# Kernel optimization log

Measured on AMD Instinct MI355X. Metric: run time of the kernel, lower is better.

## Reference

```python
import jax, jax.numpy as jnp
import numpy as np

DIM = 768
HEADS = 12
TOPK = 32


def setup_inputs() -> dict:
    key = jax.random.key(0)
    k1, k2, k3 = jax.random.split(key, 3)
    B, hw, T = 8, 576, 4
    N = hw + T * hw
    x = jax.random.normal(k1, (B, N, DIM), dtype=jnp.float32)
    qkv_w = jax.random.normal(k2, (3 * DIM, DIM), dtype=jnp.float32) * 0.02
    proj_w = jax.random.normal(k3, (DIM, DIM), dtype=jnp.float32) * 0.02
    proj_b = jnp.zeros((DIM,), dtype=jnp.float32)
    return {"x": x, "qkv_w": qkv_w, "proj_w": proj_w, "proj_b": proj_b, "T": T, "hw": hw}


def _query_topk_every_frame(attn, hw, T):
    # attn: [B, H, hw, hw + T*hw]
    B, H, n1, _ = attn.shape
    qa = attn[..., :hw]                       # [B,H,hw,hw] query self part
    ma = attn[..., hw:].reshape(B, H, n1, T, hw)  # per-frame memory scores
    vals, idx = jax.lax.top_k(ma, TOPK)       # [B,H,hw,T,K]
    cat = jnp.concatenate([qa, vals.reshape(B, H, n1, T * TOPK)], axis=-1)
    sm = jax.nn.softmax(cat, axis=-1)         # softmax over hw + T*K survivors
    qa2 = sm[..., :hw]
    tv = sm[..., hw:].reshape(B, H, n1, T, TOPK)
    # scatter normalized top-k values back into dense per-frame affinity
    bi = jnp.arange(B)[:, None, None, None, None]
    hi = jnp.arange(H)[None, :, None, None, None]
    ni = jnp.arange(n1)[None, None, :, None, None]
    ti = jnp.arange(T)[None, None, None, :, None]
    aff = jnp.zeros_like(ma).at[bi, hi, ni, ti, idx].set(tv)
    return jnp.concatenate([qa2, aff.reshape(B, H, n1, T * hw)], axis=-1)


def reference(x, qkv_w, proj_w, proj_b, T, hw):
    B, N, C = x.shape
    assert N == hw + T * hw
    hd = C // HEADS
    scale = hd ** -0.5
    qkv = (x @ qkv_w.T).reshape(B, N, 3, HEADS, hd).transpose(2, 0, 3, 1, 4)
    q, k, v = qkv[0], qkv[1], qkv[2]          # each [B,H,N,hd]
    query_q = q[:, :, :hw]                    # [B,H,hw,hd]
    attn = jnp.einsum('bhqd,bhkd->bhqk', query_q, k) * scale  # [B,H,hw,N]
    attn = _query_topk_every_frame(attn, hw, T)
    out = jnp.einsum('bhqk,bhkd->bhqd', attn, v)  # [B,H,hw,hd]
    query = out.transpose(0, 2, 1, 3).reshape(B, hw, C)
    query = query @ proj_w.T + proj_b
    # memory tokens pass through unchanged
    return jnp.concatenate([query, x[:, hw:]], axis=1)
```

## Files before the change

kernel.cpp:

```cpp
#include <hip/hip_runtime.h>
#include <hip/hip_bf16.h>


using s16x8 = __attribute__((ext_vector_type(8))) short;
using f32x4 = __attribute__((ext_vector_type(4))) float;
typedef unsigned short u16;

#define MFMA_B16(A,B,C) __builtin_amdgcn_mfma_f32_16x16x32_bf16(A,B,C,0,0,0)

__device__ __forceinline__ u16 f2bf(float f) {
  unsigned u = __float_as_uint(f);
  u += 0x7FFFu + ((u >> 16) & 1u);
  return (u16)(u >> 16);
}
__device__ __forceinline__ float bf2f(u16 h) {
  return __uint_as_float(((unsigned)h) << 16);
}
__device__ __forceinline__ int lanes_below(unsigned long long m) {
  return __builtin_amdgcn_mbcnt_hi((unsigned)(m >> 32),
         __builtin_amdgcn_mbcnt_lo((unsigned)m, 0));
}

__global__ __launch_bounds__(256) void cvt_kernel(const float* __restrict__ src,
                                                  u16* __restrict__ dst, int n4) {
  int i = blockIdx.x * blockDim.x + threadIdx.x;
  if (i >= n4) return;
  float4 v = ((const float4*)src)[i];
  unsigned lo = (unsigned)f2bf(v.x) | ((unsigned)f2bf(v.y) << 16);
  unsigned hi = (unsigned)f2bf(v.z) | ((unsigned)f2bf(v.w) << 16);
  uint2 o; o.x = lo; o.y = hi;
  ((uint2*)dst)[i] = o;
}

__global__ __launch_bounds__(256) void copy_tail_kernel(const float* __restrict__ x,
                                                        float* __restrict__ out) {
  int i = blockIdx.x * blockDim.x + threadIdx.x;
  int b = i / 442368;
  int off = i - b * 442368;
  size_t e = (size_t)b * 552960 + 110592 + off;
  ((float4*)out)[e] = ((const float4*)x)[e];
}

template<int MODE>
__global__ __launch_bounds__(256) void gemm_nt(
    const u16* __restrict__ A, const u16* __restrict__ Bw,
    const float* __restrict__ bias,
    u16* __restrict__ qbuf, u16* __restrict__ kbuf,
    u16* __restrict__ vbuf, u16* __restrict__ vtb,
    float* __restrict__ fout)
{
  constexpr int LDT = 72;
  __shared__ __align__(16) u16 sA[64 * LDT];
  __shared__ __align__(16) u16 sB[64 * LDT];
  const int n0 = blockIdx.x * 64;
  const int m0 = blockIdx.y * 64;
  if (MODE == 0) {
    if (n0 < 768 && (blockIdx.y % 45) >= 9) return;
  }
  const int tid = threadIdx.x;
  const int w = tid >> 6, lane = tid & 63;
  const int srow = tid >> 2, scb = tid & 3;
  const int mh = (w >> 1) * 32, nh = (w & 1) * 32;
  f32x4 z = {0.f, 0.f, 0.f, 0.f};
  f32x4 acc[2][2] = {{z, z}, {z, z}};

  for (int k0 = 0; k0 < 768; k0 += 64) {
    __syncthreads();
    #pragma unroll
    for (int c = scb; c < 8; c += 4) {
      *(int4*)&sA[srow * LDT + c * 8] =
          *(const int4*)&A[(size_t)(m0 + srow) * 768 + k0 + c * 8];
      *(int4*)&sB[srow * LDT + c * 8] =
          *(const int4*)&Bw[(size_t)(n0 + srow) * 768 + k0 + c * 8];
    }
    __syncthreads();
    #pragma unroll
    for (int kk = 0; kk < 2; ++kk) {
      const int ko = kk * 32 + (lane >> 4) * 8;
      s16x8 a0 = *(const s16x8*)&sA[(mh +      (lane & 15)) * LDT + ko];
      s16x8 a1 = *(const s16x8*)&sA[(mh + 16 + (lane & 15)) * LDT + ko];
      s16x8 b0 = *(const s16x8*)&sB[(nh +      (lane & 15)) * LDT + ko];
      s16x8 b1 = *(const s16x8*)&sB[(nh + 16 + (lane & 15)) * LDT + ko];
      acc[0][0] = MFMA_B16(a0, b0, acc[0][0]);
      acc[0][1] = MFMA_B16(a0, b1, acc[0][1]);
      acc[1][0] = MFMA_B16(a1, b0, acc[1][0]);
      acc[1][1] = MFMA_B16(a1, b1, acc[1][1]);
    }
  }

  if (MODE == 0) {
    const int which = n0 / 768;
    const int h = (n0 % 768) >> 6;
    #pragma unroll
    for (int mi = 0; mi < 2; ++mi)
      #pragma unroll
      for (int ni = 0; ni < 2; ++ni)
        #pragma unroll
        for (int r = 0; r < 4; ++r) {
          const int gm = m0 + mh + mi * 16 + (lane >> 4) * 4 + r;
          const int d  = nh + ni * 16 + (lane & 15);
          const int b  = gm / 2880;
          const int rr = gm - b * 2880;
          const float c = acc[mi][ni][r];
          if (which == 0) {
            if (rr < 576)
              qbuf[((size_t)(b * 12 + h) * 576 + rr) * 64 + d] = f2bf(c * 0.125f);
          } else if (which == 1) {
            kbuf[((size_t)(b * 12 + h) * 2880 + rr) * 64 + d] = f2bf(c);
          } else {
            const u16 bv = f2bf(c);
            vbuf[((size_t)(b * 12 + h) * 2880 + rr) * 64 + d] = bv;
            vtb[((size_t)((b * 12 + h) * 64 + d)) * 2880 + rr] = bv;
          }
        }
  } else {
    #pragma unroll
    for (int mi = 0; mi < 2; ++mi)
      #pragma unroll
      for (int ni = 0; ni < 2; ++ni)
        #pragma unroll
        for (int r = 0; r < 4; ++r) {
          const int gm = m0 + mh + mi * 16 + (lane >> 4) * 4 + r;
          const int gn = n0 + nh + ni * 16 + (lane & 15);
          const int b = gm / 576;
          const int q = gm - b * 576;
          fout[((size_t)b * 2880 + q) * 768 + gn] = acc[mi][ni][r] + bias[gn];
        }
  }
}

__global__ __launch_bounds__(256, 8) void attn_kernel(
    const u16* __restrict__ qbuf, const u16* __restrict__ kbuf,
    const u16* __restrict__ vbuf, const u16* __restrict__ vtb,
    u16* __restrict__ aout)
{
  constexpr int PST = 584;
  __shared__ __align__(16) u16 s_p[16 * PST];
  __shared__ float s_denom[16];

  const int bid = blockIdx.x;
  const int L = (bid & 7) * 432 + (bid >> 3);
  const int qt = L % 36;
  const int h  = (L / 36) % 12;
  const int b  = L / 432;
  const int bh = b * 12 + h;
  const int q0 = qt * 16;
  const int tid = threadIdx.x, w = tid >> 6, lane = tid & 63;
  const int l15 = lane & 15, rg = lane >> 4;
  const int ko = rg * 8;

  const u16* qp = qbuf + ((size_t)bh * 576 + q0) * 64;
  s16x8 aQ[2];
  aQ[0] = *(const s16x8*)&qp[l15 * 64 + ko];
  aQ[1] = *(const s16x8*)&qp[l15 * 64 + 32 + ko];

  const u16* kp = kbuf + (size_t)bh * 2880 * 64;
  const u16* vt = vtb + ((size_t)bh * 64 + w * 16 + l15) * 2880;
  f32x4 zz = {0.f, 0.f, 0.f, 0.f};
  f32x4 accO = zz;

  for (int c = 0; c < 5; ++c) {
    #pragma unroll 3
    for (int t = 0; t < 9; ++t) {
      const int wk = w * 144 + t * 16;
      const u16* kr = kp + (size_t)(c * 576 + wk + l15) * 64 + ko;
      s16x8 kf0 = *(const s16x8*)&kr[0];
      s16x8 kf1 = *(const s16x8*)&kr[32];
      f32x4 a0 = zz;
      a0 = MFMA_B16(aQ[0], kf0, a0);
      a0 = MFMA_B16(aQ[1], kf1, a0);
      if (c == 0) {
        #pragma unroll
        for (int r = 0; r < 4; ++r)
          s_p[(rg * 4 + r) * PST + wk + l15] = f2bf(__expf(a0[r]));
      } else {
        #pragma unroll
        for (int r = 0; r < 4; ++r)
          s_p[(rg * 4 + r) * PST + wk + l15] = f2bf(a0[r]);
      }
    }
    __syncthreads();

    if (c == 0) {
      #pragma unroll
      for (int ri = 0; ri < 4; ++ri) {
        const int q = w * 4 + ri;
        float s = 0.f;
        #pragma unroll
        for (int j = 0; j < 9; ++j) s += bf2f(s_p[q * PST + lane + 64 * j]);
        #pragma unroll
        for (int off = 1; off < 64; off <<= 1) s += __shfl_xor(s, off);
        if (lane == 0) s_denom[q] = s;
      }
    } else {
      for (int ri = 0; ri < 4; ++ri) {
        const int q = w * 4 + ri;
        unsigned key[9];
        #pragma unroll
        for (int j = 0; j < 9; ++j) {
          unsigned raw = s_p[q * PST + lane + 64 * j];
          key[j] = (raw & 0x8000u) ? (raw ^ 0xFFFFu) : (raw | 0x8000u);
        }
        unsigned prefix = 0;
        for (int bit = 15; bit >= 0; --bit) {
          const unsigned cand = prefix | (1u << bit);
          int cnt = 0;
          #pragma unroll
          for (int j = 0; j < 9; ++j)
            cnt += __popcll(__ballot(key[j] >= cand));
          if (cnt >= 32) prefix = cand;
          if (cnt == 32) break;
        }
        unsigned long long eqm[9];
        int cnt_gt = 0;
        #pragma unroll
        for (int j = 0; j < 9; ++j) {
          cnt_gt += __popcll(__ballot(key[j] > prefix));
          eqm[j] = __ballot(key[j] == prefix);
        }
        const int rem = 32 - cnt_gt;
        int run_eq = 0;
        float dsum = 0.f;
        #pragma unroll
        for (int j = 0; j < 9; ++j) {
          const unsigned kk = key[j];
          const bool sel = (kk > prefix) ||
              (kk == prefix && run_eq + lanes_below(eqm[j]) < rem);
          const u16 raw = (kk & 0x8000u) ? (u16)(kk ^ 0x8000u) : (u16)(kk ^ 0xFFFFu);
          const float e = __expf(bf2f(raw));
          const float p = sel ? e : 0.f;
          dsum += p;
          s_p[q * PST + lane + 64 * j] = f2bf(p);
          run_eq += __popcll(eqm[j]);
        }
        #pragma unroll
        for (int off = 1; off < 64; off <<= 1) dsum += __shfl_xor(dsum, off);
        if (lane == 0) s_denom[q] += dsum;
      }
      __syncthreads();
    }

    #pragma unroll 3
    for (int k0 = 0; k0 < 576; k0 += 32) {
      s16x8 vf = *(const s16x8*)&vt[c * 576 + k0 + ko];
      s16x8 pa = *(const s16x8*)&s_p[l15 * PST + k0 + ko];
      accO = MFMA_B16(pa, vf, accO);
    }
    __syncthreads();
  }

  const int d = w * 16 + l15;
  #pragma unroll
  for (int r = 0; r < 4; ++r) {
    const int row = rg * 4 + r;
    const float val = accO[r] / s_denom[row];
    aout[((size_t)(b * 576 + q0 + row)) * 768 + h * 64 + d] = f2bf(val);
  }
}

extern "C" void kernel_launch(void* const* d_in, const int* in_sizes, int n_in,
                              void* d_out, int out_size, void* d_ws, size_t ws_size,
                              hipStream_t stream)
{
  const float* x      = (const float*)d_in[0];
  const float* qkv_w  = (const float*)d_in[1];
  const float* proj_w = (const float*)d_in[2];
  const float* proj_b = (const float*)d_in[3];
  float* out = (float*)d_out;

  char* ws = (char*)d_ws;
  size_t off = 0;
  auto alloc = [&](size_t bytes) -> void* {
    void* p = ws + off;
    off += (bytes + 255) & ~(size_t)255;
    return p;
  };
  u16* xb   = (u16*)alloc((size_t)23040 * 768 * 2);
  u16* wqb  = (u16*)alloc((size_t)2304 * 768 * 2);
  u16* wpb  = (u16*)alloc((size_t)768 * 768 * 2);
  u16* qbuf = (u16*)alloc((size_t)96 * 576 * 64 * 2);
  u16* vtb  = (u16*)alloc((size_t)96 * 64 * 2880 * 2);
  u16* aout = (u16*)alloc((size_t)4608 * 768 * 2);
  u16* kbuf = (u16*)d_out;
  u16* vbuf = kbuf + (size_t)96 * 2880 * 64;

  cvt_kernel<<<17280, 256, 0, stream>>>(x, xb, 17694720 / 4);
  cvt_kernel<<<1728, 256, 0, stream>>>(qkv_w, wqb, 1769472 / 4);
  cvt_kernel<<<576, 256, 0, stream>>>(proj_w, wpb, 589824 / 4);
  gemm_nt<0><<<dim3(36, 360), 256, 0, stream>>>(xb, wqb, nullptr,
                                                qbuf, kbuf, vbuf, vtb, nullptr);
  attn_kernel<<<3456, 256, 0, stream>>>(qbuf, kbuf, vbuf, vtb, aout);
  gemm_nt<1><<<dim3(12, 72), 256, 0, stream>>>(aout, wpb, proj_b,
                                               nullptr, nullptr, nullptr, nullptr, out);
  copy_tail_kernel<<<13824, 256, 0, stream>>>(x, out);
}
```

Before: 533.8 us.

## Enlarge GEMM tiles with direct-to-LDS loads, split V transpose, streamline top-k

The GEMM moves from 64x64 to 128x128 tiles with 4x4 MFMA per wave and stages operands through global_load_lds, which raises data reuse and cuts register round-trips. The strided transposed-V store in the QKV epilogue becomes a separate LDS-based transpose kernel. The attention kernel now exponentiates every score before top-k, since exp is monotonic and positive, so keys need no sign handling. It also processes two rows per radix-select pass with no early exit and uses a permuted LDS row layout. The tradeoffs are an extra launch, more register pressure and an unpadded 64-wide LDS stride that may cause bank conflicts.

```diff
diff --git a/kernel.cpp b/kernel.cpp
--- a/kernel.cpp
+++ b/kernel.cpp
@@ -19,6 +19,11 @@
 __device__ __forceinline__ int lanes_below(unsigned long long m) {
   return __builtin_amdgcn_mbcnt_hi((unsigned)(m >> 32),
          __builtin_amdgcn_mbcnt_lo((unsigned)m, 0));
+}
+__device__ __forceinline__ void stage16(const u16* __restrict__ g, u16* l) {
+  __builtin_amdgcn_global_load_lds(
+      (const __attribute__((address_space(1))) unsigned int*)g,
+      (__attribute__((address_space(3))) unsigned int*)l, 16, 0, 0);
 }
 
 __global__ __launch_bounds__(256) void cvt_kernel(const float* __restrict__ src,
@@ -41,66 +46,96 @@
   ((float4*)out)[e] = ((const float4*)x)[e];
 }
 
+__global__ __launch_bounds__(256) void transpose_v(const u16* __restrict__ vbuf,
+                                                   u16* __restrict__ vtb) {
+  __shared__ __align__(16) u16 s[64][72];
+  const int r0 = blockIdx.x * 64;
+  const int bh = blockIdx.y;
+  const int t = threadIdx.x;
+  const int kr = t >> 2, c0 = (t & 3) * 16;
+  const u16* src = vbuf + (size_t)bh * 2880 * 64 + (size_t)(r0 + kr) * 64 + c0;
+  *(int4*)&s[kr][c0]     = *(const int4*)&src[0];
+  *(int4*)&s[kr][c0 + 8] = *(const int4*)&src[8];
+  __syncthreads();
+  const int d = t >> 2, k0 = (t & 3) * 16;
+  u16 tmp[16];
+  #pragma unroll
+  for (int i = 0; i < 16; ++i) tmp[i] = s[k0 + i][d];
+  u16* dst = vtb + ((size_t)bh * 64 + d) * 2880 + r0 + k0;
+  *(int4*)&dst[0] = *(const int4*)&tmp[0];
+  *(int4*)&dst[8] = *(const int4*)&tmp[8];
+}
+
 template<int MODE>
 __global__ __launch_bounds__(256) void gemm_nt(
     const u16* __restrict__ A, const u16* __restrict__ Bw,
     const float* __restrict__ bias,
     u16* __restrict__ qbuf, u16* __restrict__ kbuf,
-    u16* __restrict__ vbuf, u16* __restrict__ vtb,
-    float* __restrict__ fout)
+    u16* __restrict__ vbuf, float* __restrict__ fout)
 {
-  constexpr int LDT = 72;
-  __shared__ __align__(16) u16 sA[64 * LDT];
-  __shared__ __align__(16) u16 sB[64 * LDT];
-  const int n0 = blockIdx.x * 64;
-  const int m0 = blockIdx.y * 64;
-  if (MODE == 0) {
-    if (n0 < 768 && (blockIdx.y % 45) >= 9) return;
+  __shared__ __align__(16) u16 sA[128 * 64];
+  __shared__ __align__(16) u16 sB[128 * 64];
+  const int n0 = blockIdx.x * 128;
+  const int m0 = blockIdx.y * 128;
+  if (MODE == 0 && n0 < 768) {
+    const int s = m0 % 2880;
+    if (s >= 576 && s + 128 <= 2880) return;
   }
   const int tid = threadIdx.x;
   const int w = tid >> 6, lane = tid & 63;
-  const int srow = tid >> 2, scb = tid & 3;
-  const int mh = (w >> 1) * 32, nh = (w & 1) * 32;
+  const int l15 = lane & 15, rg = lane >> 4;
+  const int ko = rg * 8;
+  const int mq = (w >> 1) * 64, nq = (w & 1) * 64;
+  const int trow = tid >> 3, tcol = (tid & 7) * 8;
+
   f32x4 z = {0.f, 0.f, 0.f, 0.f};
-  f32x4 acc[2][2] = {{z, z}, {z, z}};
+  f32x4 acc[4][4];
+  #pragma unroll
+  for (int i = 0; i < 4; ++i)
+    #pragma unroll
+    for (int j = 0; j < 4; ++j) acc[i][j] = z;
 
   for (int k0 = 0; k0 < 768; k0 += 64) {
     __syncthreads();
     #pragma unroll
-    for (int c = scb; c < 8; c += 4) {
-      *(int4*)&sA[srow * LDT + c * 8] =
-          *(const int4*)&A[(size_t)(m0 + srow) * 768 + k0 + c * 8];
-      *(int4*)&sB[srow * LDT + c * 8] =
-          *(const int4*)&Bw[(size_t)(n0 + srow) * 768 + k0 + c * 8];
+    for (int i = 0; i < 4; ++i) {
+      stage16(&A[(size_t)(m0 + trow + i * 32) * 768 + k0 + tcol],
+              &sA[(trow + i * 32) * 64 + tcol]);
+      stage16(&Bw[(size_t)(n0 + trow + i * 32) * 768 + k0 + tcol],
+              &sB[(trow + i * 32) * 64 + tcol]);
     }
     __syncthreads();
     #pragma unroll
     for (int kk = 0; kk < 2; ++kk) {
-      const int ko = kk * 32 + (lane >> 4) * 8;
-      s16x8 a0 = *(const s16x8*)&sA[(mh +      (lane & 15)) * LDT + ko];
-      s16x8 a1 = *(const s16x8*)&sA[(mh + 16 + (lane & 15)) * LDT + ko];
-      s16x8 b0 = *(const s16x8*)&sB[(nh +      (lane & 15)) * LDT + ko];
-      s16x8 b1 = *(const s16x8*)&sB[(nh + 16 + (lane & 15)) * LDT + ko];
-      acc[0][0] = MFMA_B16(a0, b0, acc[0][0]);
-      acc[0][1] = MFMA_B16(a0, b1, acc[0][1]);
-      acc[1][0] = MFMA_B16(a1, b0, acc[1][0]);
-      acc[1][1] = MFMA_B16(a1, b1, acc[1][1]);
+      const int ko2 = kk * 32 + ko;
+      s16x8 af[4], bf[4];
+      #pragma unroll
+      for (int i = 0; i < 4; ++i) {
+        af[i] = *(const s16x8*)&sA[(mq + i * 16 + l15) * 64 + ko2];
+        bf[i] = *(const s16x8*)&sB[(nq + i * 16 + l15) * 64 + ko2];
+      }
+      #pragma unroll
+      for (int mi = 0; mi < 4; ++mi)
+        #pragma unroll
+        for (int ni = 0; ni < 4; ++ni)
+          acc[mi][ni] = MFMA_B16(af[mi], bf[ni], acc[mi][ni]);
     }
   }
 
   if (MODE == 0) {
     const int which = n0 / 768;
-    const int h = (n0 % 768) >> 6;
-    #pragma unroll
-    for (int mi = 0; mi < 2; ++mi)
-      #pragma unroll
-      for (int ni = 0; ni < 2; ++ni)
+    const int nb = n0 % 768;
+    #pragma unroll
+    for (int mi = 0; mi < 4; ++mi)
+      #pragma unroll
+      for (int ni = 0; ni < 4; ++ni)
         #pragma unroll
         for (int r = 0; r < 4; ++r) {
-          const int gm = m0 + mh + mi * 16 + (lane >> 4) * 4 + r;
-          const int d  = nh + ni * 16 + (lane & 15);
+          const int gm = m0 + mq + mi * 16 + rg * 4 + r;
           const int b  = gm / 2880;
           const int rr = gm - b * 2880;
+          const int ng = nb + nq + ni * 16 + l15;
+          const int h  = ng >> 6, d = ng & 63;
           const float c = acc[mi][ni][r];
           if (which == 0) {
             if (rr < 576)
@@ -108,20 +143,18 @@
           } else if (which == 1) {
             kbuf[((size_t)(b * 12 + h) * 2880 + rr) * 64 + d] = f2bf(c);
           } else {
-            const u16 bv = f2bf(c);
-            vbuf[((size_t)(b * 12 + h) * 2880 + rr) * 64 + d] = bv;
-            vtb[((size_t)((b * 12 + h) * 64 + d)) * 2880 + rr] = bv;
+            vbuf[((size_t)(b * 12 + h) * 2880 + rr) * 64 + d] = f2bf(c);
           }
         }
   } else {
     #pragma unroll
-    for (int mi = 0; mi < 2; ++mi)
-      #pragma unroll
-      for (int ni = 0; ni < 2; ++ni)
+    for (int mi = 0; mi < 4; ++mi)
+      #pragma unroll
+      for (int ni = 0; ni < 4; ++ni)
         #pragma unroll
         for (int r = 0; r < 4; ++r) {
-          const int gm = m0 + mh + mi * 16 + (lane >> 4) * 4 + r;
-          const int gn = n0 + nh + ni * 16 + (lane & 15);
+          const int gm = m0 + mq + mi * 16 + rg * 4 + r;
+          const int gn = n0 + nq + ni * 16 + l15;
           const int b = gm / 576;
           const int q = gm - b * 576;
           fout[((size_t)b * 2880 + q) * 768 + gn] = acc[mi][ni][r] + bias[gn];
@@ -131,8 +164,7 @@
 
 __global__ __launch_bounds__(256, 8) void attn_kernel(
     const u16* __restrict__ qbuf, const u16* __restrict__ kbuf,
-    const u16* __restrict__ vbuf, const u16* __restrict__ vtb,
-    u16* __restrict__ aout)
+    const u16* __restrict__ vtb, u16* __restrict__ aout)
 {
   constexpr int PST = 584;
   __shared__ __align__(16) u16 s_p[16 * PST];
@@ -156,8 +188,63 @@
 
   const u16* kp = kbuf + (size_t)bh * 2880 * 64;
   const u16* vt = vtb + ((size_t)bh * 64 + w * 16 + l15) * 2880;
+  const int prow = (((l15 & 3) << 2) | (l15 >> 2)) * PST;
   f32x4 zz = {0.f, 0.f, 0.f, 0.f};
   f32x4 accO = zz;
+
+  auto writeback = [&](int q, int lrow, const unsigned* k, unsigned prefix) {
+    unsigned long long eqm[9];
+    int cnt_gt = 0;
+    #pragma unroll
+    for (int j = 0; j < 9; ++j) {
+      unsigned long long ge = __ballot(k[j] >= prefix);
+      unsigned long long gt = __ballot(k[j] >  prefix);
+      eqm[j] = ge ^ gt;
+      cnt_gt += __popcll(gt);
+    }
+    const int rem = 32 - cnt_gt;
+    int run_eq = 0;
+    float dsum = 0.f;
+    #pragma unroll
+    for (int j = 0; j < 9; ++j) {
+      const bool isgt = k[j] > prefix;
+      const bool iseq = k[j] == prefix;
+      const bool sel = isgt || (iseq && (run_eq + lanes_below(eqm[j])) < rem);
+      const u16 raw = (u16)(k[j] & 0x7FFFu);
+      dsum += sel ? bf2f(raw) : 0.f;
+      s_p[lrow + lane + 64 * j] = sel ? raw : (u16)0;
+      run_eq += __popcll(eqm[j]);
+    }
+    #pragma unroll
+    for (int off = 1; off < 64; off <<= 1) dsum += __shfl_xor(dsum, off);
+    if (lane == 0) s_denom[q] += dsum;
+  };
+
+  auto topk2 = [&](int qA, int qB) {
+    const int lrA = ((((qA & 3) << 2) | (qA >> 2))) * PST;
+    const int lrB = ((((qB & 3) << 2) | (qB >> 2))) * PST;
+    unsigned kA[9], kB[9];
+    #pragma unroll
+    for (int j = 0; j < 9; ++j) {
+      kA[j] = (unsigned)s_p[lrA + lane + 64 * j] | 0x8000u;
+      kB[j] = (unsigned)s_p[lrB + lane + 64 * j] | 0x8000u;
+    }
+    unsigned pA = 0, pB = 0;
+    #pragma unroll
+    for (int bit = 15; bit >= 0; --bit) {
+      const unsigned cA = pA | (1u << bit), cB = pB | (1u << bit);
+      int nA = 0, nB = 0;
+      #pragma unroll
+      for (int j = 0; j < 9; ++j) {
+        nA += __popcll(__ballot(kA[j] >= cA));
+        nB += __popcll(__ballot(kB[j] >= cB));
+      }
+      pA = (nA >= 32) ? cA : pA;
+      pB = (nB >= 32) ? cB : pB;
+    }
+    writeback(qA, lrA, kA, pA);
+    writeback(qB, lrB, kB, pB);
+  };
 
   for (int c = 0; c < 5; ++c) {
     #pragma unroll 3
@@ -169,15 +256,9 @@
       f32x4 a0 = zz;
       a0 = MFMA_B16(aQ[0], kf0, a0);
       a0 = MFMA_B16(aQ[1], kf1, a0);
-      if (c == 0) {
-        #pragma unroll
-        for (int r = 0; r < 4; ++r)
-          s_p[(rg * 4 + r) * PST + wk + l15] = f2bf(__expf(a0[r]));
-      } else {
-        #pragma unroll
-        for (int r = 0; r < 4; ++r)
-          s_p[(rg * 4 + r) * PST + wk + l15] = f2bf(a0[r]);
-      }
+      #pragma unroll
+      for (int r = 0; r < 4; ++r)
+        s_p[(r * 4 + rg) * PST + wk + l15] = f2bf(__expf(a0[r]));
     }
     __syncthreads();
 
@@ -185,65 +266,24 @@
       #pragma unroll
       for (int ri = 0; ri < 4; ++ri) {
         const int q = w * 4 + ri;
+        const int lrow = (((q & 3) << 2) | (q >> 2)) * PST;
         float s = 0.f;
         #pragma unroll
-        for (int j = 0; j < 9; ++j) s += bf2f(s_p[q * PST + lane + 64 * j]);
+        for (int j = 0; j < 9; ++j) s += bf2f(s_p[lrow + lane + 64 * j]);
         #pragma unroll
         for (int off = 1; off < 64; off <<= 1) s += __shfl_xor(s, off);
         if (lane == 0) s_denom[q] = s;
       }
     } else {
-      for (int ri = 0; ri < 4; ++ri) {
-        const int q = w * 4 + ri;
-        unsigned key[9];
-        #pragma unroll
-        for (int j = 0; j < 9; ++j) {
-          unsigned raw = s_p[q * PST + lane + 64 * j];
-          key[j] = (raw & 0x8000u) ? (raw ^ 0xFFFFu) : (raw | 0x8000u);
-        }
-        unsigned prefix = 0;
-        for (int bit = 15; bit >= 0; --bit) {
-          const unsigned cand = prefix | (1u << bit);
-          int cnt = 0;
-          #pragma unroll
-          for (int j = 0; j < 9; ++j)
-            cnt += __popcll(__ballot(key[j] >= cand));
-          if (cnt >= 32) prefix = cand;
-          if (cnt == 32) break;
-        }
-        unsigned long long eqm[9];
-        int cnt_gt = 0;
-        #pragma unroll
-        for (int j = 0; j < 9; ++j) {
-          cnt_gt += __popcll(__ballot(key[j] > prefix));
-          eqm[j] = __ballot(key[j] == prefix);
-        }
-        const int rem = 32 - cnt_gt;
-        int run_eq = 0;
-        float dsum = 0.f;
-        #pragma unroll
-        for (int j = 0; j < 9; ++j) {
-          const unsigned kk = key[j];
-          const bool sel = (kk > prefix) ||
-              (kk == prefix && run_eq + lanes_below(eqm[j]) < rem);
-          const u16 raw = (kk & 0x8000u) ? (u16)(kk ^ 0x8000u) : (u16)(kk ^ 0xFFFFu);
-          const float e = __expf(bf2f(raw));
-          const float p = sel ? e : 0.f;
-          dsum += p;
-          s_p[q * PST + lane + 64 * j] = f2bf(p);
-          run_eq += __popcll(eqm[j]);
-        }
-        #pragma unroll
-        for (int off = 1; off < 64; off <<= 1) dsum += __shfl_xor(dsum, off);
-        if (lane == 0) s_denom[q] += dsum;
-      }
+      topk2(w * 4 + 0, w * 4 + 1);
+      topk2(w * 4 + 2, w * 4 + 3);
       __syncthreads();
     }
 
     #pragma unroll 3
     for (int k0 = 0; k0 < 576; k0 += 32) {
       s16x8 vf = *(const s16x8*)&vt[c * 576 + k0 + ko];
-      s16x8 pa = *(const s16x8*)&s_p[l15 * PST + k0 + ko];
+      s16x8 pa = *(const s16x8*)&s_p[prow + k0 + ko];
       accO = MFMA_B16(pa, vf, accO);
     }
     __syncthreads();
@@ -287,10 +327,11 @@
   cvt_kernel<<<17280, 256, 0, stream>>>(x, xb, 17694720 / 4);
   cvt_kernel<<<1728, 256, 0, stream>>>(qkv_w, wqb, 1769472 / 4);
   cvt_kernel<<<576, 256, 0, stream>>>(proj_w, wpb, 589824 / 4);
-  gemm_nt<0><<<dim3(36, 360), 256, 0, stream>>>(xb, wqb, nullptr,
-                                                qbuf, kbuf, vbuf, vtb, nullptr);
-  attn_kernel<<<3456, 256, 0, stream>>>(qbuf, kbuf, vbuf, vtb, aout);
-  gemm_nt<1><<<dim3(12, 72), 256, 0, stream>>>(aout, wpb, proj_b,
-                                               nullptr, nullptr, nullptr, nullptr, out);
+  gemm_nt<0><<<dim3(18, 180), 256, 0, stream>>>(xb, wqb, nullptr,
+                                                qbuf, kbuf, vbuf, nullptr);
+  transpose_v<<<dim3(45, 96), 256, 0, stream>>>(vbuf, vtb);
+  attn_kernel<<<3456, 256, 0, stream>>>(qbuf, kbuf, vtb, aout);
+  gemm_nt<1><<<dim3(6, 36), 256, 0, stream>>>(aout, wpb, proj_b,
+                                              nullptr, nullptr, nullptr, out);
   copy_tail_kernel<<<13824, 256, 0, stream>>>(x, out);
 }
```

Result: slower. 546.7 us (+2.4%).
